# Optimization experiments

Measured on AMD Instinct MI355X. Metric: run time of the kernel, lower is better.

The kernel has to match this reference:

```python
import jax, jax.numpy as jnp
import numpy as np

N_NODES = 100000
N_EDGES = 3200000
N_IN = 128
N_HID = 128
N_OUT = 64
HOP = 10


def setup_inputs() -> dict:
    key = jax.random.key(0)
    ks = jax.random.split(key, 8)
    x = jax.random.normal(ks[0], (N_NODES, N_IN), dtype=jnp.float32)
    edge_row = jax.random.randint(ks[1], (N_EDGES,), 0, N_NODES, dtype=jnp.int32)
    edge_col = jax.random.randint(ks[2], (N_EDGES,), 0, N_NODES, dtype=jnp.int32)
    # normalized-ish edge weights so 10 hops of propagation stay bounded
    edge_val = jax.random.uniform(ks[3], (N_EDGES,), dtype=jnp.float32) / 32.0
    s_ih = 1.0 / np.sqrt(N_IN)
    s_hh = 1.0 / np.sqrt(N_HID)
    W_ih = jax.random.normal(ks[4], (4 * N_HID, N_IN), dtype=jnp.float32) * s_ih
    W_hh = jax.random.normal(ks[5], (4 * N_HID, N_HID), dtype=jnp.float32) * s_hh
    b_ih = jnp.zeros((4 * N_HID,), dtype=jnp.float32)
    b_hh = jnp.zeros((4 * N_HID,), dtype=jnp.float32)
    fc_w = jax.random.normal(ks[6], (N_OUT, N_HID), dtype=jnp.float32) * s_hh
    fc_b = jnp.zeros((N_OUT,), dtype=jnp.float32)
    return dict(x=x, edge_row=edge_row, edge_col=edge_col, edge_val=edge_val,
                W_ih=W_ih, W_hh=W_hh, b_ih=b_ih, b_hh=b_hh, fc_w=fc_w, fc_b=fc_b)


def _lstm_cell(x, h, c, W_ih, W_hh, b_ih, b_hh):
    # torch LSTMCell gate order: input, forget, cell(g), output
    gates = x @ W_ih.T + b_ih + h @ W_hh.T + b_hh  # [N, 4H]
    i, f, g, o = jnp.split(gates, 4, axis=-1)
    i = jax.nn.sigmoid(i)
    f = jax.nn.sigmoid(f)
    g = jnp.tanh(g)
    o = jax.nn.sigmoid(o)
    c_new = f * c + i * g
    h_new = o * jnp.tanh(c_new)
    return h_new, c_new


def _spmm(edge_row, edge_col, edge_val, h, n_nodes):
    # (A @ h)[r] = sum_{edges e with row r} val[e] * h[col[e]]
    msgs = edge_val[:, None] * h[edge_col]  # [E, H] gather
    return jax.ops.segment_sum(msgs, edge_row, num_segments=n_nodes)


def reference(x, edge_row, edge_col, edge_val, W_ih, W_hh, b_ih, b_hh, fc_w, fc_b):
    n = x.shape[0]
    h = jnp.zeros((n, W_hh.shape[1]), dtype=x.dtype)
    c = jnp.zeros_like(h)
    # hop iterations: LSTM gate update then sparse propagation (dropout = eval/identity)
    for _ in range(HOP):
        h, c = _lstm_cell(x, h, c, W_ih, W_hh, b_ih, b_hh)
        h = _spmm(edge_row, edge_col, edge_val, h, n)
    h = jax.nn.relu(h)
    return h @ fc_w.T + fc_b
```

## Files before the change

### kernel.cpp

```cpp
#include <hip/hip_runtime.h>
#include <hip/hip_bf16.h>
#include <math.h>

constexpr int NN  = 100000;
constexpr int EE  = 3200000;
constexpr int HID = 128;
constexpr int NG  = 512;
constexpr int NOUT = 64;
constexpr int HOPS = 10;
constexpr int SCAN_BLK = 1024;
constexpr int NBLK_SCAN = (NN + SCAN_BLK - 1) / SCAN_BLK;
constexpr int NTILE = NN / 32;
constexpr int PERSIST = 256;
constexpr size_t CPERM_SLOTS = (size_t)NTILE * 4 * 2 * 2 * 64;

typedef __attribute__((ext_vector_type(8))) short short8;
typedef __attribute__((ext_vector_type(4))) float f32x4;
typedef __attribute__((ext_vector_type(4))) _Float16 half4;
typedef unsigned long long ull;

__device__ __forceinline__ ushort f2bf(float f) {
    uint u = __builtin_bit_cast(uint, f);
    u += 0x7fff + ((u >> 16) & 1);
    return (ushort)(u >> 16);
}
__device__ __forceinline__ float bflo(uint u) { return __builtin_bit_cast(float, u << 16); }
__device__ __forceinline__ float bfhi(uint u) { return __builtin_bit_cast(float, u & 0xffff0000u); }

__device__ __forceinline__ float sigf(float v) { return 1.0f / (1.0f + __expf(-v)); }
__device__ __forceinline__ float tanh_fast(float x) {
    float t = __expf(-2.0f * fabsf(x));
    float r = (1.0f - t) / (1.0f + t);
    return copysignf(r, x);
}

__device__ __forceinline__ short8 load_frag(const ushort* p) {
    return *reinterpret_cast<const short8*>(p);
}
__device__ __forceinline__ f32x4 mfma16(short8 a, short8 b, f32x4 c) {
    return __builtin_amdgcn_mfma_f32_16x16x32_bf16(a, b, c, 0, 0, 0);
}

__global__ __launch_bounds__(256) void convert_bf16_kernel(
    const float* __restrict__ src, ushort* __restrict__ dst, int n4)
{
    int i = blockIdx.x * 256 + threadIdx.x;
    if (i < n4) {
        float4 v = reinterpret_cast<const float4*>(src)[i];
        ushort4 o;
        o.x = f2bf(v.x); o.y = f2bf(v.y); o.z = f2bf(v.z); o.w = f2bf(v.w);
        reinterpret_cast<ushort4*>(dst)[i] = o;
    }
}

__global__ __launch_bounds__(256) void bsum_kernel(
    const float* __restrict__ bih, const float* __restrict__ bhh, float* __restrict__ bsum)
{
    int i = blockIdx.x * 256 + threadIdx.x;
    if (i < NG) bsum[i] = bih[i] + bhh[i];
}

__global__ __launch_bounds__(256) void hist_kernel(const int* __restrict__ erow,
                                                   int* __restrict__ deg)
{
    int e = blockIdx.x * 256 + threadIdx.x;
    atomicAdd(&deg[erow[e]], 1);
}

__global__ __launch_bounds__(SCAN_BLK) void scan1_kernel(const int* __restrict__ deg,
                                                         int* __restrict__ bsums)
{
    __shared__ int tmp[SCAN_BLK];
    int t = threadIdx.x;
    int i = blockIdx.x * SCAN_BLK + t;
    tmp[t] = (i < NN) ? deg[i] : 0;
    __syncthreads();
    for (int off = SCAN_BLK / 2; off > 0; off >>= 1) {
        if (t < off) tmp[t] += tmp[t + off];
        __syncthreads();
    }
    if (t == 0) bsums[blockIdx.x] = tmp[0];
}

__global__ __launch_bounds__(128) void scan2_kernel(int* __restrict__ bsums)
{
    __shared__ int tmp[128];
    int t = threadIdx.x;
    tmp[t] = (t < NBLK_SCAN) ? bsums[t] : 0;
    __syncthreads();
    for (int off = 1; off < 128; off <<= 1) {
        int add = (t >= off) ? tmp[t - off] : 0;
        __syncthreads();
        tmp[t] += add;
        __syncthreads();
    }
    if (t < NBLK_SCAN) bsums[t] = (t == 0) ? 0 : tmp[t - 1];
}

__global__ __launch_bounds__(SCAN_BLK) void scan3_kernel(const int* __restrict__ deg,
                                                         const int* __restrict__ bsums,
                                                         int* __restrict__ rp,
                                                         int* __restrict__ cur)
{
    __shared__ int tmp[SCAN_BLK];
    int t = threadIdx.x;
    int i = blockIdx.x * SCAN_BLK + t;
    int v = (i < NN) ? deg[i] : 0;
    tmp[t] = v;
    __syncthreads();
    for (int off = 1; off < SCAN_BLK; off <<= 1) {
        int add = (t >= off) ? tmp[t - off] : 0;
        __syncthreads();
        tmp[t] += add;
        __syncthreads();
    }
    int incl = tmp[t] + bsums[blockIdx.x];
    if (i < NN) {
        rp[i + 1] = incl;
        cur[i] = incl - v;
    }
    if (i == 0) rp[0] = 0;
}

__global__ __launch_bounds__(256) void scatter_kernel(
    const int* __restrict__ erow, const int* __restrict__ ecol,
    const float* __restrict__ eval, int* __restrict__ cur,
    int2* __restrict__ epack)
{
    int e = blockIdx.x * 256 + threadIdx.x;
    int r = erow[e];
    int p = atomicAdd(&cur[r], 1);
    int2 pk;
    pk.x = ecol[e];
    pk.y = __builtin_bit_cast(int, eval[e]);
    epack[p] = pk;
}

template<bool FIRST>
__global__ __launch_bounds__(256, 1) void cell_kernel(
    const ushort* __restrict__ xb, const ushort* __restrict__ hb,
    const ushort* __restrict__ Wib, const ushort* __restrict__ Whb,
    const float* __restrict__ bsum, half4* __restrict__ cperm,
    ushort* __restrict__ hout)
{
    __shared__ __align__(16) ushort lds_h[32 * 136];

    const int t  = threadIdx.x;
    const int l  = t & 63;
    const int w  = t >> 6;
    const int lr = l & 15;
    const int lk = l >> 4;

    short8 wi[8][4], wh[8][4];
#pragma unroll
    for (int nI = 0; nI < 8; ++nI) {
        const size_t wb = (size_t)((4 * nI + w) * 16 + lr) * HID + lk * 8;
#pragma unroll
        for (int ks = 0; ks < 4; ++ks) {
            wi[nI][ks] = load_frag(Wib + wb + ks * 32);
            if (!FIRST) wh[nI][ks] = load_frag(Whb + wb + ks * 32);
        }
    }
    float bs[8];
#pragma unroll
    for (int nI = 0; nI < 8; ++nI) bs[nI] = bsum[(4 * nI + w) * 16 + lr];

    for (int tile = blockIdx.x; tile < NTILE; tile += PERSIST) {
        const int row0 = tile * 32;

        f32x4 acc[8][2];
#pragma unroll
        for (int nI = 0; nI < 8; ++nI) {
            acc[nI][0] = f32x4{bs[nI], bs[nI], bs[nI], bs[nI]};
            acc[nI][1] = acc[nI][0];
        }

        short8 a[2][4];
#pragma unroll
        for (int rf = 0; rf < 2; ++rf) {
            const size_t ab = (size_t)(row0 + rf * 16 + lr) * HID + lk * 8;
#pragma unroll
            for (int ks = 0; ks < 4; ++ks) a[rf][ks] = load_frag(xb + ab + ks * 32);
        }
#pragma unroll
        for (int nI = 0; nI < 8; ++nI)
#pragma unroll
            for (int rf = 0; rf < 2; ++rf)
#pragma unroll
                for (int ks = 0; ks < 4; ++ks)
                    acc[nI][rf] = mfma16(a[rf][ks], wi[nI][ks], acc[nI][rf]);

        if (!FIRST) {
#pragma unroll
            for (int rf = 0; rf < 2; ++rf) {
                const size_t ab = (size_t)(row0 + rf * 16 + lr) * HID + lk * 8;
#pragma unroll
                for (int ks = 0; ks < 4; ++ks) a[rf][ks] = load_frag(hb + ab + ks * 32);
            }
#pragma unroll
            for (int nI = 0; nI < 8; ++nI)
#pragma unroll
                for (int rf = 0; rf < 2; ++rf)
#pragma unroll
                    for (int ks = 0; ks < 4; ++ks)
                        acc[nI][rf] = mfma16(a[rf][ks], wh[nI][ks], acc[nI][rf]);
        }

        __syncthreads();

#pragma unroll
        for (int nj = 0; nj < 2; ++nj) {
            const int col = (w + 4 * nj) * 16 + lr;
#pragma unroll
            for (int rf = 0; rf < 2; ++rf) {
                f32x4 iv = acc[nj][rf];
                f32x4 fv = acc[nj + 2][rf];
                f32x4 gv = acc[nj + 4][rf];
                f32x4 ov = acc[nj + 6][rf];
                const size_t cidx = ((((size_t)tile * 4 + w) * 2 + nj) * 2 + rf) * 64 + l;
                float cold[4];
                if (FIRST) {
                    cold[0] = cold[1] = cold[2] = cold[3] = 0.f;
                } else {
                    half4 ch = cperm[cidx];
#pragma unroll
                    for (int jj = 0; jj < 4; ++jj) cold[jj] = (float)ch[jj];
                }
                half4 cw;
                float hn[4];
#pragma unroll
                for (int jj = 0; jj < 4; ++jj) {
                    float c2 = sigf(fv[jj]) * cold[jj] + sigf(iv[jj]) * tanh_fast(gv[jj]);
                    cw[jj] = (_Float16)c2;
                    hn[jj] = sigf(ov[jj]) * tanh_fast(c2);
                }
                cperm[cidx] = cw;
                const int rbase = rf * 16 + lk * 4;
#pragma unroll
                for (int jj = 0; jj < 4; ++jj)
                    lds_h[(rbase + jj) * 136 + col] = f2bf(hn[jj]);
            }
        }
        __syncthreads();
        {
            const ushort* lsrc = &lds_h[(t >> 3) * 136 + (t & 7) * 16];
            short8 v0 = *reinterpret_cast<const short8*>(lsrc);
            short8 v1 = *reinterpret_cast<const short8*>(lsrc + 8);
            ushort* gdst = hout + (size_t)row0 * HID + t * 16;
            *reinterpret_cast<short8*>(gdst) = v0;
            *reinterpret_cast<short8*>(gdst + 8) = v1;
        }
    }
}

__global__ __launch_bounds__(256) void spmm_kernel(
    const int* __restrict__ rp, const int2* __restrict__ epack,
    const ushort* __restrict__ hin, ushort* __restrict__ hout)
{
    int r = blockIdx.x * 4 + (threadIdx.x >> 6);
    if (r >= NN) return;
    int l = threadIdx.x & 63;
    int beg = rp[r], end = rp[r + 1];
    const ull* eq = reinterpret_cast<const ull*>(epack);

    float s0a = 0.f, s1a = 0.f, s0b = 0.f, s1b = 0.f;
    float s0c = 0.f, s1c = 0.f, s0d = 0.f, s1d = 0.f;
    int e = beg;
    for (; e + 4 <= end; e += 4) {
        ull u0 = __builtin_nontemporal_load(eq + e);
        ull u1 = __builtin_nontemporal_load(eq + e + 1);
        ull u2 = __builtin_nontemporal_load(eq + e + 2);
        ull u3 = __builtin_nontemporal_load(eq + e + 3);
        int c0 = (int)(uint)u0, c1 = (int)(uint)u1, c2 = (int)(uint)u2, c3 = (int)(uint)u3;
        float v0 = __builtin_bit_cast(float, (uint)(u0 >> 32));
        float v1 = __builtin_bit_cast(float, (uint)(u1 >> 32));
        float v2 = __builtin_bit_cast(float, (uint)(u2 >> 32));
        float v3 = __builtin_bit_cast(float, (uint)(u3 >> 32));
        uint g0 = *reinterpret_cast<const uint*>(hin + (size_t)c0 * HID + l * 2);
        uint g1 = *reinterpret_cast<const uint*>(hin + (size_t)c1 * HID + l * 2);
        uint g2 = *reinterpret_cast<const uint*>(hin + (size_t)c2 * HID + l * 2);
        uint g3 = *reinterpret_cast<const uint*>(hin + (size_t)c3 * HID + l * 2);
        s0a += v0 * bflo(g0); s1a += v0 * bfhi(g0);
        s0b += v1 * bflo(g1); s1b += v1 * bfhi(g1);
        s0c += v2 * bflo(g2); s1c += v2 * bfhi(g2);
        s0d += v3 * bflo(g3); s1d += v3 * bfhi(g3);
    }
    for (; e < end; ++e) {
        ull u0 = __builtin_nontemporal_load(eq + e);
        int c0 = (int)(uint)u0;
        float v0 = __builtin_bit_cast(float, (uint)(u0 >> 32));
        uint g0 = *reinterpret_cast<const uint*>(hin + (size_t)c0 * HID + l * 2);
        s0a += v0 * bflo(g0); s1a += v0 * bfhi(g0);
    }
    float s0 = (s0a + s0b) + (s0c + s0d);
    float s1 = (s1a + s1b) + (s1c + s1d);
    uint o = ((uint)f2bf(s1) << 16) | (uint)f2bf(s0);
    *reinterpret_cast<uint*>(hout + (size_t)r * HID + l * 2) = o;
}

__global__ __launch_bounds__(256) void final_mfma_kernel(
    const ushort* __restrict__ hb, const ushort* __restrict__ fcwb,
    const float* __restrict__ fcb, float* __restrict__ out)
{
    const int t = threadIdx.x;
    const int l = t & 63;
    const int w = t >> 6;
    const int lr = l & 15;
    const int lk = l >> 4;
    const int row0 = blockIdx.x * 64 + w * 16;

    f32x4 acc[4];
#pragma unroll
    for (int n = 0; n < 4; ++n) {
        float b = fcb[n * 16 + lr];
        acc[n] = f32x4{b, b, b, b};
    }

    const short8 z8 = {0, 0, 0, 0, 0, 0, 0, 0};
    const int arow = row0 + lr;
    const bool aok = arow < NN;
    short8 a[4];
#pragma unroll
    for (int ks = 0; ks < 4; ++ks) {
        short8 v = aok ? load_frag(hb + (size_t)arow * HID + ks * 32 + lk * 8) : z8;
#pragma unroll
        for (int i = 0; i < 8; ++i) {
            ushort u = (ushort)v[i];
            if (u & 0x8000) v[i] = 0;
        }
        a[ks] = v;
    }

#pragma unroll
    for (int n = 0; n < 4; ++n) {
        const ushort* wp = fcwb + (size_t)(n * 16 + lr) * HID + lk * 8;
#pragma unroll
        for (int ks = 0; ks < 4; ++ks)
            acc[n] = mfma16(a[ks], load_frag(wp + ks * 32), acc[n]);
    }

#pragma unroll
    for (int n = 0; n < 4; ++n) {
#pragma unroll
        for (int j = 0; j < 4; ++j) {
            int row = row0 + lk * 4 + j;
            if (row < NN) out[(size_t)row * NOUT + n * 16 + lr] = acc[n][j];
        }
    }
}

extern "C" void kernel_launch(void* const* d_in, const int* in_sizes, int n_in,
                              void* d_out, int out_size, void* d_ws, size_t ws_size,
                              hipStream_t stream)
{
    const float* x    = (const float*)d_in[0];
    const int*   erow = (const int*)d_in[1];
    const int*   ecol = (const int*)d_in[2];
    const float* eval = (const float*)d_in[3];
    const float* Wih  = (const float*)d_in[4];
    const float* Whh  = (const float*)d_in[5];
    const float* bih  = (const float*)d_in[6];
    const float* bhh  = (const float*)d_in[7];
    const float* fcw  = (const float*)d_in[8];
    const float* fcb  = (const float*)d_in[9];
    float* out = (float*)d_out;

    char* ws = (char*)d_ws;
    size_t off = 0;
    auto alloc = [&](size_t bytes) -> void* {
        void* p = ws + off;
        off = (off + bytes + 255) & ~(size_t)255;
        return p;
    };
    ushort* hb_a  = (ushort*)alloc((size_t)NN * HID * 2);
    ushort* hb_b  = (ushort*)alloc((size_t)NN * HID * 2);
    half4*  cperm = (half4*)alloc(CPERM_SLOTS * 8);
    ushort* xb    = (ushort*)alloc((size_t)NN * HID * 2);
    ushort* Wib   = (ushort*)alloc((size_t)NG * HID * 2);
    ushort* Whb   = (ushort*)alloc((size_t)NG * HID * 2);
    ushort* fcwb  = (ushort*)alloc((size_t)NOUT * HID * 2);
    float*  bsum  = (float*)alloc((size_t)NG * 4);
    int*    rp    = (int*)alloc((size_t)(NN + 1) * 4);
    int*    deg   = (int*)alloc((size_t)NN * 4);
    int*    cur   = (int*)alloc((size_t)NN * 4);
    int*    bsums = (int*)alloc((size_t)NBLK_SCAN * 4);
    int2*   epack = (int2*)alloc((size_t)EE * 8);
    (void)ws_size;

    convert_bf16_kernel<<<(NN * HID / 4 + 255) / 256, 256, 0, stream>>>(x, xb, NN * HID / 4);
    convert_bf16_kernel<<<(NG * HID / 4 + 255) / 256, 256, 0, stream>>>(Wih, Wib, NG * HID / 4);
    convert_bf16_kernel<<<(NG * HID / 4 + 255) / 256, 256, 0, stream>>>(Whh, Whb, NG * HID / 4);
    convert_bf16_kernel<<<(NOUT * HID / 4 + 255) / 256, 256, 0, stream>>>(fcw, fcwb, NOUT * HID / 4);
    bsum_kernel<<<2, 256, 0, stream>>>(bih, bhh, bsum);

    hipMemsetAsync(deg, 0, (size_t)NN * 4, stream);
    hist_kernel<<<EE / 256, 256, 0, stream>>>(erow, deg);
    scan1_kernel<<<NBLK_SCAN, SCAN_BLK, 0, stream>>>(deg, bsums);
    scan2_kernel<<<1, 128, 0, stream>>>(bsums);
    scan3_kernel<<<NBLK_SCAN, SCAN_BLK, 0, stream>>>(deg, bsums, rp, cur);
    scatter_kernel<<<EE / 256, 256, 0, stream>>>(erow, ecol, eval, cur, epack);

    const int SPMM_GRID = NN / 4;

    cell_kernel<true><<<PERSIST, 256, 0, stream>>>(xb, hb_b, Wib, Whb, bsum, cperm, hb_a);
    spmm_kernel<<<SPMM_GRID, 256, 0, stream>>>(rp, epack, hb_a, hb_b);
    for (int hop = 1; hop < HOPS; ++hop) {
        cell_kernel<false><<<PERSIST, 256, 0, stream>>>(xb, hb_b, Wib, Whb, bsum, cperm, hb_a);
        spmm_kernel<<<SPMM_GRID, 256, 0, stream>>>(rp, epack, hb_a, hb_b);
    }

    final_mfma_kernel<<<(NN + 63) / 64, 256, 0, stream>>>(hb_b, fcwb, fcb, out);
}
```

Baseline: 2.743 ms.

## Split LSTM cell gate columns across eight waves per block instead of four

The persistent cell kernel now launches 512 threads (8 waves) per block, with each wave owning one 16-column slice of hidden units across all four gates. This halves the register-resident weight fragments and accumulators per wave, raising occupancy to two blocks per CU, and simplifies the gate epilogue and the LDS-to-global store. The intent is to hide load latency in the gate GEMM with more resident waves, at the cost of more waves sharing each tile's A-fragment loads and barriers.

```diff
diff --git a/kernel.cpp b/kernel.cpp
--- a/kernel.cpp
+++ b/kernel.cpp
@@ -12,7 +12,7 @@
 constexpr int NBLK_SCAN = (NN + SCAN_BLK - 1) / SCAN_BLK;
 constexpr int NTILE = NN / 32;
 constexpr int PERSIST = 256;
-constexpr size_t CPERM_SLOTS = (size_t)NTILE * 4 * 2 * 2 * 64;
+constexpr size_t CPERM_SLOTS = (size_t)NTILE * 8 * 2 * 64;
 
 typedef __attribute__((ext_vector_type(8))) short short8;
 typedef __attribute__((ext_vector_type(4))) float f32x4;
@@ -137,7 +137,7 @@
 }
 
 template<bool FIRST>
-__global__ __launch_bounds__(256, 1) void cell_kernel(
+__global__ __launch_bounds__(512, 2) void cell_kernel(
     const ushort* __restrict__ xb, const ushort* __restrict__ hb,
     const ushort* __restrict__ Wib, const ushort* __restrict__ Whb,
     const float* __restrict__ bsum, half4* __restrict__ cperm,
@@ -151,28 +151,30 @@
     const int lr = l & 15;
     const int lk = l >> 4;
 
-    short8 wi[8][4], wh[8][4];
-#pragma unroll
-    for (int nI = 0; nI < 8; ++nI) {
-        const size_t wb = (size_t)((4 * nI + w) * 16 + lr) * HID + lk * 8;
+    short8 wi[4][4], wh[4][4];
+#pragma unroll
+    for (int gI = 0; gI < 4; ++gI) {
+        const size_t wb = (size_t)((w + 8 * gI) * 16 + lr) * HID + lk * 8;
 #pragma unroll
         for (int ks = 0; ks < 4; ++ks) {
-            wi[nI][ks] = load_frag(Wib + wb + ks * 32);
-            if (!FIRST) wh[nI][ks] = load_frag(Whb + wb + ks * 32);
-        }
-    }
-    float bs[8];
-#pragma unroll
-    for (int nI = 0; nI < 8; ++nI) bs[nI] = bsum[(4 * nI + w) * 16 + lr];
+            wi[gI][ks] = load_frag(Wib + wb + ks * 32);
+            if (!FIRST) wh[gI][ks] = load_frag(Whb + wb + ks * 32);
+        }
+    }
+    float bs[4];
+#pragma unroll
+    for (int gI = 0; gI < 4; ++gI) bs[gI] = bsum[(w + 8 * gI) * 16 + lr];
+
+    const int col = w * 16 + lr;
 
     for (int tile = blockIdx.x; tile < NTILE; tile += PERSIST) {
         const int row0 = tile * 32;
 
-        f32x4 acc[8][2];
-#pragma unroll
-        for (int nI = 0; nI < 8; ++nI) {
-            acc[nI][0] = f32x4{bs[nI], bs[nI], bs[nI], bs[nI]};
-            acc[nI][1] = acc[nI][0];
+        f32x4 acc[4][2];
+#pragma unroll
+        for (int gI = 0; gI < 4; ++gI) {
+            acc[gI][0] = f32x4{bs[gI], bs[gI], bs[gI], bs[gI]};
+            acc[gI][1] = acc[gI][0];
         }
 
         short8 a[2][4];
@@ -183,12 +185,12 @@
             for (int ks = 0; ks < 4; ++ks) a[rf][ks] = load_frag(xb + ab + ks * 32);
         }
 #pragma unroll
-        for (int nI = 0; nI < 8; ++nI)
+        for (int gI = 0; gI < 4; ++gI)
 #pragma unroll
             for (int rf = 0; rf < 2; ++rf)
 #pragma unroll
                 for (int ks = 0; ks < 4; ++ks)
-                    acc[nI][rf] = mfma16(a[rf][ks], wi[nI][ks], acc[nI][rf]);
+                    acc[gI][rf] = mfma16(a[rf][ks], wi[gI][ks], acc[gI][rf]);
 
         if (!FIRST) {
 #pragma unroll
@@ -198,57 +200,50 @@
                 for (int ks = 0; ks < 4; ++ks) a[rf][ks] = load_frag(hb + ab + ks * 32);
             }
 #pragma unroll
-            for (int nI = 0; nI < 8; ++nI)
+            for (int gI = 0; gI < 4; ++gI)
 #pragma unroll
                 for (int rf = 0; rf < 2; ++rf)
 #pragma unroll
                     for (int ks = 0; ks < 4; ++ks)
-                        acc[nI][rf] = mfma16(a[rf][ks], wh[nI][ks], acc[nI][rf]);
-        }
-
-        __syncthreads();
-
-#pragma unroll
-        for (int nj = 0; nj < 2; ++nj) {
-            const int col = (w + 4 * nj) * 16 + lr;
-#pragma unroll
-            for (int rf = 0; rf < 2; ++rf) {
-                f32x4 iv = acc[nj][rf];
-                f32x4 fv = acc[nj + 2][rf];
-                f32x4 gv = acc[nj + 4][rf];
-                f32x4 ov = acc[nj + 6][rf];
-                const size_t cidx = ((((size_t)tile * 4 + w) * 2 + nj) * 2 + rf) * 64 + l;
-                float cold[4];
-                if (FIRST) {
-                    cold[0] = cold[1] = cold[2] = cold[3] = 0.f;
-                } else {
-                    half4 ch = cperm[cidx];
-#pragma unroll
-                    for (int jj = 0; jj < 4; ++jj) cold[jj] = (float)ch[jj];
-                }
-                half4 cw;
-                float hn[4];
-#pragma unroll
-                for (int jj = 0; jj < 4; ++jj) {
-                    float c2 = sigf(fv[jj]) * cold[jj] + sigf(iv[jj]) * tanh_fast(gv[jj]);
-                    cw[jj] = (_Float16)c2;
-                    hn[jj] = sigf(ov[jj]) * tanh_fast(c2);
-                }
-                cperm[cidx] = cw;
-                const int rbase = rf * 16 + lk * 4;
-#pragma unroll
-                for (int jj = 0; jj < 4; ++jj)
-                    lds_h[(rbase + jj) * 136 + col] = f2bf(hn[jj]);
+                        acc[gI][rf] = mfma16(a[rf][ks], wh[gI][ks], acc[gI][rf]);
+        }
+
+        __syncthreads();
+
+#pragma unroll
+        for (int rf = 0; rf < 2; ++rf) {
+            f32x4 iv = acc[0][rf];
+            f32x4 fv = acc[1][rf];
+            f32x4 gv = acc[2][rf];
+            f32x4 ov = acc[3][rf];
+            const size_t cidx = (((size_t)tile * 8 + w) * 2 + rf) * 64 + l;
+            float cold[4];
+            if (FIRST) {
+                cold[0] = cold[1] = cold[2] = cold[3] = 0.f;
+            } else {
+                half4 ch = cperm[cidx];
+#pragma unroll
+                for (int jj = 0; jj < 4; ++jj) cold[jj] = (float)ch[jj];
             }
+            half4 cw;
+            float hn[4];
+#pragma unroll
+            for (int jj = 0; jj < 4; ++jj) {
+                float c2 = sigf(fv[jj]) * cold[jj] + sigf(iv[jj]) * tanh_fast(gv[jj]);
+                cw[jj] = (_Float16)c2;
+                hn[jj] = sigf(ov[jj]) * tanh_fast(c2);
+            }
+            cperm[cidx] = cw;
+            const int rbase = rf * 16 + lk * 4;
+#pragma unroll
+            for (int jj = 0; jj < 4; ++jj)
+                lds_h[(rbase + jj) * 136 + col] = f2bf(hn[jj]);
         }
         __syncthreads();
         {
-            const ushort* lsrc = &lds_h[(t >> 3) * 136 + (t & 7) * 16];
-            short8 v0 = *reinterpret_cast<const short8*>(lsrc);
-            short8 v1 = *reinterpret_cast<const short8*>(lsrc + 8);
-            ushort* gdst = hout + (size_t)row0 * HID + t * 16;
-            *reinterpret_cast<short8*>(gdst) = v0;
-            *reinterpret_cast<short8*>(gdst + 8) = v1;
+            short8 v = *reinterpret_cast<const short8*>(
+                &lds_h[(t >> 4) * 136 + (t & 15) * 8]);
+            *reinterpret_cast<short8*>(hout + (size_t)row0 * HID + t * 8) = v;
         }
     }
 }
@@ -402,10 +397,10 @@
 
     const int SPMM_GRID = NN / 4;
 
-    cell_kernel<true><<<PERSIST, 256, 0, stream>>>(xb, hb_b, Wib, Whb, bsum, cperm, hb_a);
+    cell_kernel<true><<<PERSIST, 512, 0, stream>>>(xb, hb_b, Wib, Whb, bsum, cperm, hb_a);
     spmm_kernel<<<SPMM_GRID, 256, 0, stream>>>(rp, epack, hb_a, hb_b);
     for (int hop = 1; hop < HOPS; ++hop) {
-        cell_kernel<false><<<PERSIST, 256, 0, stream>>>(xb, hb_b, Wib, Whb, bsum, cperm, hb_a);
+        cell_kernel<false><<<PERSIST, 512, 0, stream>>>(xb, hb_b, Wib, Whb, bsum, cperm, hb_a);
         spmm_kernel<<<SPMM_GRID, 256, 0, stream>>>(rp, epack, hb_a, hb_b);
     }
 
```

Measured after the change: 2.747 ms. No clear change (+0.1%).
